# Performance work log

Hardware: AMD Instinct MI355X
Metric: run time of the kernel (lower is better)

Reference implementation:

```python
import jax, jax.numpy as jnp
import numpy as np

DIM = 1024
NUM_HEADS = 16
HEAD_DIM = DIM // NUM_HEADS
SCALE = HEAD_DIM ** -0.5


def setup_inputs() -> dict:
    key = jax.random.key(0)
    k_x, k_wq, k_bq, k_wp, k_bp = jax.random.split(key, 5)
    x = jax.random.normal(k_x, (2, 2048, DIM), dtype=jnp.float32)
    # torch Linear weights: [out_features, in_features]
    W_qkv = jax.random.normal(k_wq, (3 * DIM, DIM), dtype=jnp.float32) * (DIM ** -0.5)
    b_qkv = jax.random.normal(k_bq, (3 * DIM,), dtype=jnp.float32) * 0.02
    W_proj = jax.random.normal(k_wp, (DIM, DIM), dtype=jnp.float32) * (DIM ** -0.5)
    b_proj = jax.random.normal(k_bp, (DIM,), dtype=jnp.float32) * 0.02
    return {"x": x, "W_qkv": W_qkv, "b_qkv": b_qkv, "W_proj": W_proj, "b_proj": b_proj}


def reference(x, W_qkv, b_qkv, W_proj, b_proj):
    B, N, C = x.shape
    qkv = x @ W_qkv.T + b_qkv                      # [B, N, 3C]
    q, k, v = jnp.split(qkv, 3, axis=-1)           # each [B, N, C]
    def heads(t):
        return t.reshape(B, N, NUM_HEADS, HEAD_DIM).transpose(0, 2, 1, 3)  # [B,H,N,D]
    q, k, v = heads(q), heads(k), heads(v)
    attn = jnp.einsum('bhnd,bhmd->bhnm', q, k) * SCALE
    attn = jax.nn.softmax(attn, axis=-1)
    out = jnp.einsum('bhnm,bhmd->bhnd', attn, v)   # [B,H,N,D]
    out = out.transpose(0, 2, 1, 3).reshape(B, N, C)
    return out @ W_proj.T + b_proj
```

## Files before the change

### kernel.cpp

```cpp
#include <hip/hip_runtime.h>


typedef unsigned short u16;
typedef __attribute__((ext_vector_type(8))) _Float16 f16x8;
typedef __attribute__((ext_vector_type(2))) __fp16 fp16x2;
typedef __attribute__((ext_vector_type(4))) float f32x4;

#define DEV static __device__ __forceinline__
#define MFMA16(a, b, c) __builtin_amdgcn_mfma_f32_16x16x32_f16(a, b, c, 0, 0, 0)

DEV u16 f2h(float f) { _Float16 h = (_Float16)f; return __builtin_bit_cast(u16, h); }
DEV float h2f(u16 u) { return (float)__builtin_bit_cast(_Float16, u); }
DEV unsigned pkrtz(float a, float b) {
  fp16x2 h2 = __builtin_amdgcn_cvt_pkrtz(a, b);
  return __builtin_bit_cast(unsigned, h2);
}

DEV void async16(u16* dst, const u16* src) {
  __builtin_amdgcn_global_load_lds(
      (const __attribute__((address_space(1))) unsigned int*)(const void*)src,
      (__attribute__((address_space(3))) unsigned int*)(void*)dst, 16, 0, 0);
}

__global__ __launch_bounds__(256) void k_split_all(
    const float* __restrict__ x, const float* __restrict__ wq,
    const float* __restrict__ wp, u16* __restrict__ xh,
    u16* __restrict__ wqh, u16* __restrict__ wph) {
  int i = blockIdx.x * 256 + threadIdx.x;
  const float* src;
  u16* dh;
  int off;
  if (i < 1048576) { src = x;  dh = xh;  off = i; }
  else if (i < 1835008) { src = wq; dh = wqh; off = i - 1048576; }
  else { src = wp; dh = wph; off = i - 1835008; }
  float4 v = ((const float4*)src)[off];
  ushort4 h;
  h.x = f2h(v.x); h.y = f2h(v.y); h.z = f2h(v.z); h.w = f2h(v.w);
  ((ushort4*)dh)[off] = h;
}

__global__ __launch_bounds__(512) void k_gemmq(
    const u16* __restrict__ Ah_g, const u16* __restrict__ Bh_g,
    const float* __restrict__ bias,
    u16* __restrict__ oQh, u16* __restrict__ oKh, u16* __restrict__ oVh) {
  __shared__ u16 lds[40960];
  const int t = threadIdx.x;
  const int lane = t & 63, g = lane >> 4, cl = lane & 15;
  const int w = t >> 6;
  const int mi = blockIdx.x >> 4, ni = blockIdx.x & 15;
  const int m0 = mi * 128, n0 = ni * 192;
  const int wr = (w >> 1) * 32, wc = (w & 1) * 96;

  f32x4 acc[2][6] = {};

#define STAGE_AB(kt_, pb_)                                                  \
  {                                                                         \
    const int k0__ = (kt_) * 64;                                            \
    const unsigned pb__ = (pb_);                                            \
    _Pragma("unroll") for (int j = 0; j < 5; ++j) {                         \
      int gs = j * 512 + t;                                                 \
      const u16* src;                                                       \
      if (gs < 1024) {                                                      \
        int row = gs >> 3;                                                  \
        int c = (gs & 7) ^ (row & 7);                                       \
        src = Ah_g + (m0 + row) * 1024 + k0__ + c * 8;                      \
      } else {                                                              \
        int s = gs - 1024;                                                  \
        int row = s >> 3;                                                   \
        int c = (s & 7) ^ (row & 7);                                        \
        src = Bh_g + (n0 + row) * 1024 + k0__ + c * 8;                      \
      }                                                                     \
      async16(&lds[pb__ + (unsigned)(gs & ~63) * 8], src);                  \
    }                                                                       \
  }

#define COMPUTE_TILE(base_)                                                 \
  {                                                                         \
    const unsigned base__ = (base_);                                        \
    _Pragma("unroll") for (int ks = 0; ks < 2; ++ks) {                      \
      f16x8 af[2], bfr[6];                                                  \
      _Pragma("unroll") for (int fm = 0; fm < 2; ++fm) {                    \
        int rowL = wr + fm * 16 + cl;                                       \
        unsigned idx = base__ + rowL * 64 + (((4 * ks + g) ^ (rowL & 7)) * 8); \
        af[fm] = *(const f16x8*)&lds[idx];                                  \
      }                                                                     \
      _Pragma("unroll") for (int fn = 0; fn < 6; ++fn) {                    \
        int rowL = wc + fn * 16 + cl;                                       \
        unsigned idx = base__ + 8192 + rowL * 64 +                          \
                       (((4 * ks + g) ^ (rowL & 7)) * 8);                   \
        bfr[fn] = *(const f16x8*)&lds[idx];                                 \
      }                                                                     \
      _Pragma("unroll") for (int fm = 0; fm < 2; ++fm)                      \
        _Pragma("unroll") for (int fn = 0; fn < 6; ++fn)                    \
          acc[fm][fn] = MFMA16(af[fm], bfr[fn], acc[fm][fn]);               \
    }                                                                       \
  }

  STAGE_AB(0, 0u);
  STAGE_AB(1, 20480u);

  for (int kt = 0; kt < 15; ++kt) {
    asm volatile("s_waitcnt vmcnt(5)" ::: "memory");
    __builtin_amdgcn_sched_barrier(0);
    __builtin_amdgcn_s_barrier();
    __builtin_amdgcn_sched_barrier(0);
    const unsigned base = (kt & 1) ? 20480u : 0u;
    COMPUTE_TILE(base);
    asm volatile("s_waitcnt lgkmcnt(0)" ::: "memory");
    __builtin_amdgcn_sched_barrier(0);
    __builtin_amdgcn_s_barrier();
    __builtin_amdgcn_sched_barrier(0);
    if (kt < 14) STAGE_AB(kt + 2, base);
  }
  asm volatile("s_waitcnt vmcnt(0)" ::: "memory");
  __builtin_amdgcn_sched_barrier(0);
  __builtin_amdgcn_s_barrier();
  __builtin_amdgcn_sched_barrier(0);
  COMPUTE_TILE(20480u);
#undef STAGE_AB
#undef COMPUTE_TILE

#pragma unroll
  for (int fm = 0; fm < 2; ++fm) {
#pragma unroll
    for (int fn = 0; fn < 6; ++fn) {
      int cc = n0 + wc + fn * 16 + cl;
      float bv = bias[cc];
      f32x4 a = acc[fm][fn];
#pragma unroll
      for (int r = 0; r < 4; ++r) {
        int rr = m0 + wr + fm * 16 + g * 4 + r;
        float v = a[r] + bv;
        int seg = cc >> 10, cm = cc & 1023;
        int h = cm >> 6, d = cm & 63;
        int b = rr >> 11, n = rr & 2047;
        int bh = b * 16 + h;
        if (seg == 0) {
          v *= 0.1803368801111204f;
          oQh[(bh * 2048 + n) * 64 + d] = f2h(v);
        } else if (seg == 1) {
          oKh[(bh * 2048 + n) * 64 + d] = f2h(v);
        } else {
          oVh[(bh * 64 + d) * 2048 + n] = f2h(v);
        }
      }
    }
  }
}

__global__ __launch_bounds__(512) void k_gemm(
    const u16* __restrict__ Ah_g, const u16* __restrict__ Bh_g,
    const float* __restrict__ bias, float* __restrict__ fout, int nbn) {
  __shared__ u16 lds[32768];
  const int t = threadIdx.x;
  const int lane = t & 63, g = lane >> 4, cl = lane & 15;
  const int w = t >> 6;
  const int mi = blockIdx.x / nbn, ni = blockIdx.x % nbn;
  const int m0 = mi * 128, n0 = ni * 128;
  const int wr = (w >> 1) * 32, wc = (w & 1) * 64;

  f32x4 acc[2][4] = {};

#define STAGE_AB(kt_, pb_)                                                  \
  {                                                                         \
    const int k0__ = (kt_) * 64;                                            \
    const unsigned pb__ = (pb_);                                            \
    _Pragma("unroll") for (int j = 0; j < 4; ++j) {                         \
      int gs = j * 512 + t;                                                 \
      int tensor = gs >> 10;                                                \
      int s = gs & 1023;                                                    \
      int row = s >> 3;                                                     \
      int c = (s & 7) ^ (row & 7);                                          \
      const u16* src = tensor ? Bh_g + (n0 + row) * 1024 + k0__ + c * 8     \
                              : Ah_g + (m0 + row) * 1024 + k0__ + c * 8;    \
      async16(&lds[pb__ + (unsigned)(gs & ~63) * 8], src);                  \
    }                                                                       \
  }

#define COMPUTE_TILE(base_)                                                 \
  {                                                                         \
    const unsigned base__ = (base_);                                        \
    _Pragma("unroll") for (int ks = 0; ks < 2; ++ks) {                      \
      f16x8 af[2], bfr[4];                                                  \
      _Pragma("unroll") for (int fm = 0; fm < 2; ++fm) {                    \
        int rowL = wr + fm * 16 + cl;                                       \
        unsigned idx = base__ + rowL * 64 + (((4 * ks + g) ^ (rowL & 7)) * 8); \
        af[fm] = *(const f16x8*)&lds[idx];                                  \
      }                                                                     \
      _Pragma("unroll") for (int fn = 0; fn < 4; ++fn) {                    \
        int rowL = wc + fn * 16 + cl;                                       \
        unsigned idx = base__ + 8192 + rowL * 64 +                          \
                       (((4 * ks + g) ^ (rowL & 7)) * 8);                   \
        bfr[fn] = *(const f16x8*)&lds[idx];                                 \
      }                                                                     \
      _Pragma("unroll") for (int fm = 0; fm < 2; ++fm)                      \
        _Pragma("unroll") for (int fn = 0; fn < 4; ++fn)                    \
          acc[fm][fn] = MFMA16(af[fm], bfr[fn], acc[fm][fn]);               \
    }                                                                       \
  }

  STAGE_AB(0, 0u);
  STAGE_AB(1, 16384u);

  for (int kt = 0; kt < 15; ++kt) {
    asm volatile("s_waitcnt vmcnt(4)" ::: "memory");
    __builtin_amdgcn_sched_barrier(0);
    __builtin_amdgcn_s_barrier();
    __builtin_amdgcn_sched_barrier(0);
    const unsigned base = (kt & 1) ? 16384u : 0u;
    COMPUTE_TILE(base);
    asm volatile("s_waitcnt lgkmcnt(0)" ::: "memory");
    __builtin_amdgcn_sched_barrier(0);
    __builtin_amdgcn_s_barrier();
    __builtin_amdgcn_sched_barrier(0);
    if (kt < 14) STAGE_AB(kt + 2, base);
  }
  asm volatile("s_waitcnt vmcnt(0)" ::: "memory");
  __builtin_amdgcn_sched_barrier(0);
  __builtin_amdgcn_s_barrier();
  __builtin_amdgcn_sched_barrier(0);
  COMPUTE_TILE(16384u);
#undef STAGE_AB
#undef COMPUTE_TILE

#pragma unroll
  for (int fm = 0; fm < 2; ++fm) {
#pragma unroll
    for (int fn = 0; fn < 4; ++fn) {
      int cc = n0 + wc + fn * 16 + cl;
      float bv = bias[cc];
      f32x4 a = acc[fm][fn];
#pragma unroll
      for (int r = 0; r < 4; ++r) {
        int rr = m0 + wr + fm * 16 + g * 4 + r;
        fout[rr * 1024 + cc] = a[r] + bv;
      }
    }
  }
}

__global__ __launch_bounds__(512, 4) void k_attn(
    const u16* __restrict__ Qh, const u16* __restrict__ Kh,
    const u16* __restrict__ Vh, u16* __restrict__ Oh) {
  __shared__ u16 lds[40960];
  const int t = threadIdx.x, w = t >> 6, lane = t & 63, g = lane >> 4, cl = lane & 15;
  int bid = (blockIdx.x & 7) * 64 + (blockIdx.x >> 3);
  const int bh = bid >> 4, qt = bid & 15;
  const int n0 = qt * 128;
  const int PH = 32768 + w * 1024;

  f16x8 qf[2];
  {
    int rg = bh * 2048 + n0 + w * 16 + cl;
#pragma unroll
    for (int ks = 0; ks < 2; ++ks)
      qf[ks] = *(const f16x8*)&Qh[rg * 64 + ks * 32 + g * 8];
  }

  f32x4 o[4] = {};
  f32x4 ps4 = {0.f, 0.f, 0.f, 0.f};
  const int bsrc = (lane & 48) | ((lane >> 2) & 12);
  const int swz = (cl & 7) << 3;

#define STAGE_KV2(kts_, pbase_)                                            \
  {                                                                        \
    const int kt2__ = 2 * (kts_);                                          \
    const unsigned pb__ = (pbase_);                                        \
    _Pragma("unroll") for (int j = 0; j < 4; ++j) {                        \
      int gs = j * 512 + t;                                                \
      int tensor = gs >> 9, s = gs & 511, row = s >> 3;                    \
      int c = (s & 7) ^ (row & 7);                                         \
      int sub = tensor >> 1;                                               \
      const u16* src;                                                      \
      if ((tensor & 1) == 0)                                               \
        src = Kh + (bh * 2048 + (kt2__ + sub) * 64 + row) * 64 + c * 8;    \
      else                                                                 \
        src = Vh + (bh * 64 + row) * 2048 + (kt2__ + sub) * 64 + c * 8;    \
      async16(&lds[pb__ + (unsigned)(gs & ~63) * 8], src);                 \
    }                                                                      \
  }

#define COMPUTE_KV(base_)                                                   \
  {                                                                         \
    const unsigned base__ = (base_);                                        \
    f32x4 st[4] = {};                                                       \
    __builtin_amdgcn_s_setprio(1);                                          \
    _Pragma("unroll") for (int fn = 0; fn < 4; ++fn) {                      \
      int krow = fn * 16 + cl;                                              \
      _Pragma("unroll") for (int ks = 0; ks < 2; ++ks) {                    \
        unsigned idx = base__ + krow * 64 + (((4 * ks + g) ^ (krow & 7)) * 8); \
        f16x8 kf = *(const f16x8*)&lds[idx];                                \
        st[fn] = MFMA16(kf, qf[ks], st[fn]);                                \
      }                                                                     \
    }                                                                       \
    __builtin_amdgcn_s_setprio(0);                                          \
    unsigned upk[4][2];                                                     \
    _Pragma("unroll") for (int fn = 0; fn < 4; ++fn) {                      \
      float p0 = __builtin_amdgcn_exp2f(st[fn][0]);                         \
      float p1 = __builtin_amdgcn_exp2f(st[fn][1]);                         \
      float p2 = __builtin_amdgcn_exp2f(st[fn][2]);                         \
      float p3 = __builtin_amdgcn_exp2f(st[fn][3]);                         \
      ps4[0] += p0; ps4[1] += p1; ps4[2] += p2; ps4[3] += p3;               \
      upk[fn][0] = pkrtz(p0, p1);                                           \
      upk[fn][1] = pkrtz(p2, p3);                                           \
    }                                                                       \
    _Pragma("unroll") for (int fn = 0; fn < 4; ++fn) {                      \
      int addr = (cl * 64 + fn * 16 + 4 * g) ^ swz;                         \
      *(uint2*)&lds[PH + addr] = make_uint2(upk[fn][0], upk[fn][1]);        \
    }                                                                       \
    f16x8 pa[2];                                                            \
    _Pragma("unroll") for (int ks = 0; ks < 2; ++ks) {                      \
      int addr = (cl * 64 + ks * 32 + 8 * g) ^ swz;                         \
      pa[ks] = *(const f16x8*)&lds[PH + addr];                              \
    }                                                                       \
    __builtin_amdgcn_s_setprio(1);                                          \
    _Pragma("unroll") for (int fd = 0; fd < 4; ++fd) {                      \
      int vrow = fd * 16 + cl;                                              \
      _Pragma("unroll") for (int ks = 0; ks < 2; ++ks) {                    \
        unsigned idx = base__ + 4096 + vrow * 64 +                          \
                       (((4 * ks + g) ^ (vrow & 7)) * 8);                   \
        f16x8 vf = *(const f16x8*)&lds[idx];                                \
        o[fd] = MFMA16(pa[ks], vf, o[fd]);                                  \
      }                                                                     \
    }                                                                       \
    __builtin_amdgcn_s_setprio(0);                                          \
  }

  STAGE_KV2(0, 0u);
  STAGE_KV2(1, 16384u);

  for (int kts = 0; kts < 15; ++kts) {
    asm volatile("s_waitcnt vmcnt(4)" ::: "memory");
    __builtin_amdgcn_sched_barrier(0);
    __builtin_amdgcn_s_barrier();
    __builtin_amdgcn_sched_barrier(0);
    const unsigned base = (kts & 1) ? 16384u : 0u;
    COMPUTE_KV(base);
    COMPUTE_KV(base + 8192u);
    asm volatile("s_waitcnt lgkmcnt(0)" ::: "memory");
    __builtin_amdgcn_sched_barrier(0);
    __builtin_amdgcn_s_barrier();
    __builtin_amdgcn_sched_barrier(0);
    if (kts < 14) STAGE_KV2(kts + 2, base);
  }
  asm volatile("s_waitcnt vmcnt(0)" ::: "memory");
  __builtin_amdgcn_sched_barrier(0);
  __builtin_amdgcn_s_barrier();
  __builtin_amdgcn_sched_barrier(0);
  COMPUTE_KV(16384u);
  COMPUTE_KV(16384u + 8192u);
#undef STAGE_KV2
#undef COMPUTE_KV

  float lrun = (ps4[0] + ps4[1]) + (ps4[2] + ps4[3]);
  lrun += __shfl_xor(lrun, 16);
  lrun += __shfl_xor(lrun, 32);
  const int b = bh >> 4, h = bh & 15;
  float l0 = __shfl(lrun, bsrc), l1 = __shfl(lrun, bsrc | 1);
  float l2 = __shfl(lrun, bsrc | 2), l3 = __shfl(lrun, bsrc | 3);
  float inv[4] = {1.0f / l0, 1.0f / l1, 1.0f / l2, 1.0f / l3};
#pragma unroll
  for (int fd = 0; fd < 4; ++fd)
#pragma unroll
    for (int r = 0; r < 4; ++r) {
      float v = o[fd][r] * inv[r];
      int rowg = b * 2048 + n0 + w * 16 + 4 * g + r;
      int colg = h * 64 + fd * 16 + cl;
      Oh[rowg * 1024 + colg] = f2h(v);
    }
}

extern "C" void kernel_launch(void* const* d_in, const int* in_sizes, int n_in,
                              void* d_out, int out_size, void* d_ws, size_t ws_size,
                              hipStream_t stream) {
  const float* x  = (const float*)d_in[0];
  const float* Wq = (const float*)d_in[1];
  const float* bq = (const float*)d_in[2];
  const float* Wp = (const float*)d_in[3];
  const float* bp = (const float*)d_in[4];
  float* out = (float*)d_out;
  char* ws = (char*)d_ws;

  u16* Xh  = (u16*)(ws + 0);
  u16* Wqh = (u16*)(ws + 8388608);
  u16* Wph = (u16*)(ws + 14680064);
  u16* Qh  = (u16*)(ws + 16777216);
  u16* Kh  = (u16*)(ws + 25165824);
  u16* Vh  = (u16*)(ws + 33554432);

  k_split_all<<<8192, 256, 0, stream>>>(x, Wq, Wp, Xh, Wqh, Wph);

  k_gemmq<<<512, 512, 0, stream>>>(Xh, Wqh, bq, Qh, Kh, Vh);
  k_attn<<<512, 512, 0, stream>>>(Qh, Kh, Vh, Xh);
  k_gemm<<<32 * 8, 512, 0, stream>>>(Xh, Wph, bp, out, 8);
}
```

Measured before the change: 122.1 us.

## Double attention query rows per wave and shrink projection GEMM tiles

The attention kernel now gives each wave 32 query rows instead of 16, so each block covers 256 queries and each K/V fragment loaded from LDS feeds two MFMAs. This halves the grid to 256 blocks and raises register and LDS use. The output projection GEMM switches to 64x128 tiles with 512 blocks, so the grid covers the CUs more evenly. Both changes trade reuse against occupancy and parallelism: the attention grid is now exactly 256 blocks, and the occupancy hint (launch_bounds min blocks) is dropped.

New measurement: 120.6 us, median of 3. No clear change (-1.2%).

```diff
diff --git a/kernel.cpp b/kernel.cpp
--- a/kernel.cpp
+++ b/kernel.cpp
@@ -53,7 +53,7 @@
 
   f32x4 acc[2][6] = {};
 
-#define STAGE_AB(kt_, pb_)                                                  \
+#define STAGE_ABQ(kt_, pb_)                                                 \
   {                                                                         \
     const int k0__ = (kt_) * 64;                                            \
     const unsigned pb__ = (pb_);                                            \
@@ -74,7 +74,7 @@
     }                                                                       \
   }
 
-#define COMPUTE_TILE(base_)                                                 \
+#define COMPUTE_TILEQ(base_)                                                \
   {                                                                         \
     const unsigned base__ = (base_);                                        \
     _Pragma("unroll") for (int ks = 0; ks < 2; ++ks) {                      \
@@ -96,8 +96,8 @@
     }                                                                       \
   }
 
-  STAGE_AB(0, 0u);
-  STAGE_AB(1, 20480u);
+  STAGE_ABQ(0, 0u);
+  STAGE_ABQ(1, 20480u);
 
   for (int kt = 0; kt < 15; ++kt) {
     asm volatile("s_waitcnt vmcnt(5)" ::: "memory");
@@ -105,20 +105,20 @@
     __builtin_amdgcn_s_barrier();
     __builtin_amdgcn_sched_barrier(0);
     const unsigned base = (kt & 1) ? 20480u : 0u;
-    COMPUTE_TILE(base);
+    COMPUTE_TILEQ(base);
     asm volatile("s_waitcnt lgkmcnt(0)" ::: "memory");
     __builtin_amdgcn_sched_barrier(0);
     __builtin_amdgcn_s_barrier();
     __builtin_amdgcn_sched_barrier(0);
-    if (kt < 14) STAGE_AB(kt + 2, base);
+    if (kt < 14) STAGE_ABQ(kt + 2, base);
   }
   asm volatile("s_waitcnt vmcnt(0)" ::: "memory");
   __builtin_amdgcn_sched_barrier(0);
   __builtin_amdgcn_s_barrier();
   __builtin_amdgcn_sched_barrier(0);
-  COMPUTE_TILE(20480u);
-#undef STAGE_AB
-#undef COMPUTE_TILE
+  COMPUTE_TILEQ(20480u);
+#undef STAGE_ABQ
+#undef COMPUTE_TILEQ
 
 #pragma unroll
   for (int fm = 0; fm < 2; ++fm) {
@@ -150,83 +150,88 @@
 
 __global__ __launch_bounds__(512) void k_gemm(
     const u16* __restrict__ Ah_g, const u16* __restrict__ Bh_g,
-    const float* __restrict__ bias, float* __restrict__ fout, int nbn) {
-  __shared__ u16 lds[32768];
+    const float* __restrict__ bias, float* __restrict__ fout) {
+  __shared__ u16 lds[24576];
   const int t = threadIdx.x;
   const int lane = t & 63, g = lane >> 4, cl = lane & 15;
   const int w = t >> 6;
-  const int mi = blockIdx.x / nbn, ni = blockIdx.x % nbn;
-  const int m0 = mi * 128, n0 = ni * 128;
-  const int wr = (w >> 1) * 32, wc = (w & 1) * 64;
-
-  f32x4 acc[2][4] = {};
-
-#define STAGE_AB(kt_, pb_)                                                  \
+  const int mi = blockIdx.x >> 3, ni = blockIdx.x & 7;
+  const int m0 = mi * 64, n0 = ni * 128;
+  const int wr = (w >> 2) * 32, wc = (w & 3) * 32;
+
+  f32x4 acc[2][2] = {};
+
+#define STAGE_ABP(kt_, pb_)                                                 \
   {                                                                         \
     const int k0__ = (kt_) * 64;                                            \
     const unsigned pb__ = (pb_);                                            \
-    _Pragma("unroll") for (int j = 0; j < 4; ++j) {                         \
+    _Pragma("unroll") for (int j = 0; j < 3; ++j) {                         \
       int gs = j * 512 + t;                                                 \
-      int tensor = gs >> 10;                                                \
-      int s = gs & 1023;                                                    \
-      int row = s >> 3;                                                     \
-      int c = (s & 7) ^ (row & 7);                                          \
-      const u16* src = tensor ? Bh_g + (n0 + row) * 1024 + k0__ + c * 8     \
-                              : Ah_g + (m0 + row) * 1024 + k0__ + c * 8;    \
+      const u16* src;                                                       \
+      if (gs < 512) {                                                       \
+        int row = gs >> 3;                                                  \
+        int c = (gs & 7) ^ (row & 7);                                       \
+        src = Ah_g + (m0 + row) * 1024 + k0__ + c * 8;                      \
+      } else {                                                              \
+        int s = gs - 512;                                                   \
+        int row = s >> 3;                                                   \
+        int c = (s & 7) ^ (row & 7);                                        \
+        src = Bh_g + (n0 + row) * 1024 + k0__ + c * 8;                      \
+      }                                                                     \
       async16(&lds[pb__ + (unsigned)(gs & ~63) * 8], src);                  \
     }                                                                       \
   }
 
-#define COMPUTE_TILE(base_)                                                 \
+#define COMPUTE_TILEP(base_)                                                \
   {                                                                         \
     const unsigned base__ = (base_);                                        \
     _Pragma("unroll") for (int ks = 0; ks < 2; ++ks) {                      \
-      f16x8 af[2], bfr[4];                                                  \
+      f16x8 af[2], bfr[2];                                                  \
       _Pragma("unroll") for (int fm = 0; fm < 2; ++fm) {                    \
         int rowL = wr + fm * 16 + cl;                                       \
         unsigned idx = base__ + rowL * 64 + (((4 * ks + g) ^ (rowL & 7)) * 8); \
         af[fm] = *(const f16x8*)&lds[idx];                                  \
       }                                                                     \
-      _Pragma("unroll") for (int fn = 0; fn < 4; ++fn) {                    \
+      _Pragma("unroll") for (int fn = 0; fn < 2; ++fn) {                    \
         int rowL = wc + fn * 16 + cl;                                       \
-        unsigned idx = base__ + 8192 + rowL * 64 +                          \
+        unsigned idx = base__ + 4096 + rowL * 64 +                          \
                        (((4 * ks + g) ^ (rowL & 7)) * 8);                   \
         bfr[fn] = *(const f16x8*)&lds[idx];                                 \
       }                                                                     \
       _Pragma("unroll") for (int fm = 0; fm < 2; ++fm)                      \
-        _Pragma("unroll") for (int fn = 0; fn < 4; ++fn)                    \
+        _Pragma("unroll") for (int fn = 0; fn < 2; ++fn)                    \
           acc[fm][fn] = MFMA16(af[fm], bfr[fn], acc[fm][fn]);               \
     }                                                                       \
   }
 
-  STAGE_AB(0, 0u);
-  STAGE_AB(1, 16384u);
+  STAGE_ABP(0, 0u);
+  STAGE_ABP(1, 12288u);
 
   for (int kt = 0; kt < 15; ++kt) {
-    asm volatile("s_waitcnt vmcnt(4)" ::: "memory");
-    __builtin_amdgcn_sched_barrier(0);
-    __builtin_amdgcn_s_barrier();
-    __builtin_amdgcn_sched_barrier(0);
-    const unsigned base = (kt & 1) ? 16384u : 0u;
-    COMPUTE_TILE(base);
+    asm volatile("s_waitcnt vmcnt(3)" ::: "memory");
+    __builtin_amdgcn_sched_barrier(0);
+    __builtin_amdgcn_s_barrier();
+    __builtin_amdgcn_sched_barrier(0);
+    const unsigned base = (kt & 1) ? 12288u : 0u;
+    COMPUTE_TILEP(base);
     asm volatile("s_waitcnt lgkmcnt(0)" ::: "memory");
     __builtin_amdgcn_sched_barrier(0);
     __builtin_amdgcn_s_barrier();
     __builtin_amdgcn_sched_barrier(0);
-    if (kt < 14) STAGE_AB(kt + 2, base);
+    if (kt < 14) STAGE_ABP(kt + 2, base);
   }
   asm volatile("s_waitcnt vmcnt(0)" ::: "memory");
   __builtin_amdgcn_sched_barrier(0);
   __builtin_amdgcn_s_barrier();
   __builtin_amdgcn_sched_barrier(0);
-  COMPUTE_TILE(16384u);
-#undef STAGE_AB
-#undef COMPUTE_TILE
+  COMPUTE_TILEP(12288u);
+#undef STAGE_ABP
+#undef COMPUTE_TILEP
 
 #pragma unroll
   for (int fm = 0; fm < 2; ++fm) {
 #pragma unroll
-    for (int fn = 0; fn < 4; ++fn) {
+    for (int fn = 0; fn < 2; ++fn) {
       int cc = n0 + wc + fn * 16 + cl;
       float bv = bias[cc];
       f32x4 a = acc[fm][fn];
@@ -239,28 +244,28 @@
   }
 }
 
-__global__ __launch_bounds__(512, 4) void k_attn(
+__global__ __launch_bounds__(512) void k_attn(
     const u16* __restrict__ Qh, const u16* __restrict__ Kh,
     const u16* __restrict__ Vh, u16* __restrict__ Oh) {
-  __shared__ u16 lds[40960];
+  __shared__ u16 lds[49152];
   const int t = threadIdx.x, w = t >> 6, lane = t & 63, g = lane >> 4, cl = lane & 15;
-  int bid = (blockIdx.x & 7) * 64 + (blockIdx.x >> 3);
-  const int bh = bid >> 4, qt = bid & 15;
-  const int n0 = qt * 128;
-  const int PH = 32768 + w * 1024;
-
-  f16x8 qf[2];
-  {
-    int rg = bh * 2048 + n0 + w * 16 + cl;
+  int bid = (blockIdx.x & 7) * 32 + (blockIdx.x >> 3);
+  const int bh = bid >> 3, qt = bid & 7;
+  const int n0 = qt * 256;
+  const int PH = 32768 + w * 2048;
+
+  f16x8 qf[2][2];
+#pragma unroll
+  for (int fm = 0; fm < 2; ++fm) {
+    int rg = bh * 2048 + n0 + w * 32 + fm * 16 + cl;
 #pragma unroll
     for (int ks = 0; ks < 2; ++ks)
-      qf[ks] = *(const f16x8*)&Qh[rg * 64 + ks * 32 + g * 8];
-  }
-
-  f32x4 o[4] = {};
-  f32x4 ps4 = {0.f, 0.f, 0.f, 0.f};
+      qf[fm][ks] = *(const f16x8*)&Qh[rg * 64 + ks * 32 + g * 8];
+  }
+
+  f32x4 o[2][4] = {};
+  f32x4 ps4[2] = {{0.f, 0.f, 0.f, 0.f}, {0.f, 0.f, 0.f, 0.f}};
   const int bsrc = (lane & 48) | ((lane >> 2) & 12);
-  const int swz = (cl & 7) << 3;
 
 #define STAGE_KV2(kts_, pbase_)                                            \
   {                                                                        \
@@ -283,35 +288,45 @@
 #define COMPUTE_KV(base_)                                                   \
   {                                                                         \
     const unsigned base__ = (base_);                                        \
-    f32x4 st[4] = {};                                                       \
+    f32x4 st[2][4] = {};                                                    \
     __builtin_amdgcn_s_setprio(1);                                          \
     _Pragma("unroll") for (int fn = 0; fn < 4; ++fn) {                      \
       int krow = fn * 16 + cl;                                              \
       _Pragma("unroll") for (int ks = 0; ks < 2; ++ks) {                    \
         unsigned idx = base__ + krow * 64 + (((4 * ks + g) ^ (krow & 7)) * 8); \
         f16x8 kf = *(const f16x8*)&lds[idx];                                \
-        st[fn] = MFMA16(kf, qf[ks], st[fn]);                                \
+        _Pragma("unroll") for (int fm = 0; fm < 2; ++fm)                    \
+          st[fm][fn] = MFMA16(kf, qf[fm][ks], st[fm][fn]);                  \
       }                                                                     \
     }                                                                       \
     __builtin_amdgcn_s_setprio(0);                                          \
-    unsigned upk[4][2];                                                     \
-    _Pragma("unroll") for (int fn = 0; fn < 4; ++fn) {                      \
-      float p0 = __builtin_amdgcn_exp2f(st[fn][0]);                         \
-      float p1 = __builtin_amdgcn_exp2f(st[fn][1]);                         \
-      float p2 = __builtin_amdgcn_exp2f(st[fn][2]);                         \
-      float p3 = __builtin_amdgcn_exp2f(st[fn][3]);                         \
-      ps4[0] += p0; ps4[1] += p1; ps4[2] += p2; ps4[3] += p3;               \
-      upk[fn][0] = pkrtz(p0, p1);                                           \
-      upk[fn][1] = pkrtz(p2, p3);                                           \
-    }                                                                       \
-    _Pragma("unroll") for (int fn = 0; fn < 4; ++fn) {                      \
-      int addr = (cl * 64 + fn * 16 + 4 * g) ^ swz;                         \
-      *(uint2*)&lds[PH + addr] = make_uint2(upk[fn][0], upk[fn][1]);        \
-    }                                                                       \
-    f16x8 pa[2];                                                            \
-    _Pragma("unroll") for (int ks = 0; ks < 2; ++ks) {                      \
-      int addr = (cl * 64 + ks * 32 + 8 * g) ^ swz;                         \
-      pa[ks] = *(const f16x8*)&lds[PH + addr];                              \
+    _Pragma("unroll") for (int fm = 0; fm < 2; ++fm) {                      \
+      unsigned upk[4][2];                                                   \
+      _Pragma("unroll") for (int fn = 0; fn < 4; ++fn) {                    \
+        float p0 = __builtin_amdgcn_exp2f(st[fm][fn][0]);                   \
+        float p1 = __builtin_amdgcn_exp2f(st[fm][fn][1]);                   \
+        float p2 = __builtin_amdgcn_exp2f(st[fm][fn][2]);                   \
+        float p3 = __builtin_amdgcn_exp2f(st[fm][fn][3]);                   \
+        ps4[fm][0] += p0; ps4[fm][1] += p1;                                 \
+        ps4[fm][2] += p2; ps4[fm][3] += p3;                                 \
+        upk[fn][0] = pkrtz(p0, p1);                                         \
+        upk[fn][1] = pkrtz(p2, p3);                                         \
+      }                                                                     \
+      int rq = fm * 16 + cl;                                                \
+      int swz2 = (rq & 7) << 3;                                             \
+      _Pragma("unroll") for (int fn = 0; fn < 4; ++fn) {                    \
+        int addr = (rq * 64 + fn * 16 + 4 * g) ^ swz2;                      \
+        *(uint2*)&lds[PH + addr] = make_uint2(upk[fn][0], upk[fn][1]);      \
+      }                                                                     \
+    }                                                                       \
+    f16x8 pa[2][2];                                                         \
+    _Pragma("unroll") for (int fm = 0; fm < 2; ++fm) {                      \
+      int rq = fm * 16 + cl;                                                \
+      int swz2 = (rq & 7) << 3;                                             \
+      _Pragma("unroll") for (int ks = 0; ks < 2; ++ks) {                    \
+        int addr = (rq * 64 + ks * 32 + 8 * g) ^ swz2;                      \
+        pa[fm][ks] = *(const f16x8*)&lds[PH + addr];                        \
+      }                                                                     \
     }                                                                       \
     __builtin_amdgcn_s_setprio(1);                                          \
     _Pragma("unroll") for (int fd = 0; fd < 4; ++fd) {                      \
@@ -320,7 +335,8 @@
         unsigned idx = base__ + 4096 + vrow * 64 +                          \
                        (((4 * ks + g) ^ (vrow & 7)) * 8);                   \
         f16x8 vf = *(const f16x8*)&lds[idx];                                \
-        o[fd] = MFMA16(pa[ks], vf, o[fd]);                                  \
+        _Pragma("unroll") for (int fm = 0; fm < 2; ++fm)                    \
+          o[fm][fd] = MFMA16(pa[fm][ks], vf, o[fm][fd]);                    \
       }                                                                     \
     }                                                                       \
     __builtin_amdgcn_s_setprio(0);                                          \
@@ -352,22 +368,25 @@
 #undef STAGE_KV2
 #undef COMPUTE_KV
 
-  float lrun = (ps4[0] + ps4[1]) + (ps4[2] + ps4[3]);
-  lrun += __shfl_xor(lrun, 16);
-  lrun += __shfl_xor(lrun, 32);
   const int b = bh >> 4, h = bh & 15;
-  float l0 = __shfl(lrun, bsrc), l1 = __shfl(lrun, bsrc | 1);
-  float l2 = __shfl(lrun, bsrc | 2), l3 = __shfl(lrun, bsrc | 3);
-  float inv[4] = {1.0f / l0, 1.0f / l1, 1.0f / l2, 1.0f / l3};
-#pragma unroll
-  for (int fd = 0; fd < 4; ++fd)
-#pragma unroll
-    for (int r = 0; r < 4; ++r) {
-      float v = o[fd][r] * inv[r];
-      int rowg = b * 2048 + n0 + w * 16 + 4 * g + r;
-      int colg = h * 64 + fd * 16 + cl;
-      Oh[rowg * 1024 + colg] = f2h(v);
-    }
+#pragma unroll
+  for (int fm = 0; fm < 2; ++fm) {
+    float lrun = (ps4[fm][0] + ps4[fm][1]) + (ps4[fm][2] + ps4[fm][3]);
+    lrun += __shfl_xor(lrun, 16);
+    lrun += __shfl_xor(lrun, 32);
+    float l0 = __shfl(lrun, bsrc), l1 = __shfl(lrun, bsrc | 1);
+    float l2 = __shfl(lrun, bsrc | 2), l3 = __shfl(lrun, bsrc | 3);
+    float inv[4] = {1.0f / l0, 1.0f / l1, 1.0f / l2, 1.0f / l3};
+#pragma unroll
+    for (int fd = 0; fd < 4; ++fd)
+#pragma unroll
+      for (int r = 0; r < 4; ++r) {
+        float v = o[fm][fd][r] * inv[r];
+        int rowg = b * 2048 + n0 + w * 32 + fm * 16 + 4 * g + r;
+        int colg = h * 64 + fd * 16 + cl;
+        Oh[rowg * 1024 + colg] = f2h(v);
+      }
+  }
 }
 
 extern "C" void kernel_launch(void* const* d_in, const int* in_sizes, int n_in,
@@ -391,6 +410,6 @@
   k_split_all<<<8192, 256, 0, stream>>>(x, Wq, Wp, Xh, Wqh, Wph);
 
   k_gemmq<<<512, 512, 0, stream>>>(Xh, Wqh, bq, Qh, Kh, Vh);
-  k_attn<<<512, 512, 0, stream>>>(Qh, Kh, Vh, Xh);
-  k_gemm<<<32 * 8, 512, 0, stream>>>(Xh, Wph, bp, out, 8);
-}
+  k_attn<<<256, 512, 0, stream>>>(Qh, Kh, Vh, Xh);
+  k_gemm<<<512, 512, 0, stream>>>(Xh, Wph, bp, out);
+}
```
